# Optimization experiments

Measured on AMD Instinct MI355X. Metric: run time of the kernel, lower is better.

Reference implementation:

```python
import jax, jax.numpy as jnp
import numpy as np

B, C1, C2, N1, N2 = 8, 16, 32, 256, 128


def _masks():
    # static numpy masks, mirroring EquivariantLayer.__init__
    n_max, n_min = max(N1, N2), min(N1, N2)
    k = np.arange(n_max)
    k[k > n_max // 2] -= n_max
    mask = np.abs(k) <= n_min / 2            # |k| <= n_min/2 (both nyquists)
    mask2 = mask[: n_max // 2 + 1].copy()    # taken BEFORE removing neg nyquist
    nyq_pos = k == n_min / 2
    nyq_pos2 = nyq_pos[: n_max // 2 + 1]
    nyq_neg = k == -n_min / 2
    mask[nyq_neg] = False                    # drop negative nyquist row
    return mask, mask2, nyq_pos, nyq_pos2

MASK, MASK2, NYQ_POS, NYQ_POS2 = _masks()


def rot90_kernel(t):
    # 90-deg rotation about grid point [0,0] for periodic kernels:
    # transpose last two dims, keep column 0, reverse remaining columns
    t = jnp.swapaxes(t, -1, -2)
    return jnp.concatenate([t[..., :1], t[..., 1:][..., ::-1]], axis=-1)


def symmetric_kernel(kernel):
    # average over the 8 elements of D4 (rotations + transpose*rotations)
    k1 = kernel
    k2 = rot90_kernel(k1)
    k3 = rot90_kernel(k2)
    k4 = rot90_kernel(k3)
    k5 = jnp.swapaxes(k1, -1, -2)
    k6 = rot90_kernel(k5)
    k7 = rot90_kernel(k6)
    k8 = rot90_kernel(k7)
    return (k1 + k2 + k3 + k4 + k5 + k6 + k7 + k8) / 8.0


def _forward(f, kernel):
    F = jnp.fft.rfft2(f)                                  # [b,c1,N1,N1//2+1]
    # downsample: zero nyquist modes, truncate spectrum, rescale
    F = jnp.where(jnp.asarray(NYQ_POS)[None, None, :, None], 0, F)
    F = jnp.where(jnp.asarray(NYQ_POS2)[None, None, None, :], 0, F)
    F = F[:, :, MASK, :][:, :, :, MASK2] * (N2 / N1) ** 2  # [b,c1,N2,N2//2+1]
    # spectral convolution with D4-symmetrized kernel
    K = jnp.fft.rfft2(symmetric_kernel(kernel))            # [1,c1,c2,N2,N2//2+1]
    conv = jnp.einsum('bcnk,cdnk->bdnk', F, K[0])          # sum over input channels
    return jnp.fft.irfft2(F), jnp.fft.irfft2(conv)


def setup_inputs() -> dict:
    key = jax.random.key(0)
    kf, kk = jax.random.split(key)
    f = jax.random.normal(kf, (B, C1, N1, N1), dtype=jnp.float32)
    eps = 0.1
    kernel = eps * (2.0 * jax.random.uniform(kk, (1, C1, C2, N2, N2), dtype=jnp.float32) - 1.0)
    return {"f": f, "kernel": kernel}


def reference(f, kernel):
    return _forward(f, kernel)
```

## Files before the change

### kernel.cpp

```cpp
#include <hip/hip_runtime.h>

#define PI_F 3.14159265358979f

typedef unsigned int  uint32;
typedef unsigned short ushort16;

__device__ __forceinline__ float2 cmul(float2 a, float2 b) {
    return make_float2(a.x * b.x - a.y * b.y, a.x * b.y + a.y * b.x);
}
__device__ __forceinline__ float2 cadd(float2 a, float2 b) { return make_float2(a.x + b.x, a.y + b.y); }
__device__ __forceinline__ float2 csub(float2 a, float2 b) { return make_float2(a.x - b.x, a.y - b.y); }
__device__ __forceinline__ float2 shflx(float2 v, int m) {
    return make_float2(__shfl_xor(v.x, m, 64), __shfl_xor(v.y, m, 64));
}
__device__ __forceinline__ float2 shfli(float2 v, int src) {
    return make_float2(__shfl(v.x, src, 64), __shfl(v.y, src, 64));
}
__device__ __forceinline__ int brev6(int x) { return (int)(__brev((unsigned)x) >> 26); }

__device__ __forceinline__ uint32 bfu(float x) {
    uint32 u = __float_as_uint(x);
    return (u + 0x7FFFu + ((u >> 16) & 1u)) >> 16;
}
__device__ __forceinline__ uint32 packbf2(float2 v) { return bfu(v.x) | (bfu(v.y) << 16); }
__device__ __forceinline__ float2 unpackbf2(uint32 u) {
    return make_float2(__uint_as_float(u << 16), __uint_as_float(u & 0xFFFF0000u));
}
__device__ __forceinline__ float bf2f(ushort16 u) { return __uint_as_float((uint32)u << 16); }

template<int CTRL>
__device__ __forceinline__ float dpp1(float x) {
    return __builtin_bit_cast(float, __builtin_amdgcn_update_dpp(
        0, __builtin_bit_cast(int, x), CTRL, 0xF, 0xF, true));
}
template<int CTRL>
__device__ __forceinline__ float2 dppx(float2 v) {
    return make_float2(dpp1<CTRL>(v.x), dpp1<CTRL>(v.y));
}

__device__ __forceinline__ float swz4(float x) {
    return __int_as_float(__builtin_amdgcn_ds_swizzle(__float_as_int(x), 0x101F));
}

template<bool INV>
__device__ __forceinline__ void tw_init(int lane, float2* w, float* sg) {
#pragma unroll
    for (int t = 0; t < 6; ++t) {
        int m = 32 >> t;
        bool up = (lane & m) != 0;
        int pos = lane & (m - 1);
        float ang = (INV ? PI_F : -PI_F) * (float)pos / (float)m;
        float sn, cs;
        __sincosf(ang, &sn, &cs);
        w[t]  = up ? make_float2(cs, sn) : make_float2(1.f, 0.f);
        sg[t] = (t < 2) ? (up ? -2.f : 0.f) : (up ? -1.f : 1.f);
    }
}

__device__ __forceinline__ float2 fft64s(float2 v, const float2* w, const float* sg) {
#if __has_builtin(__builtin_amdgcn_permlane32_swap) && __has_builtin(__builtin_amdgcn_permlane16_swap)
    {
        auto rx = __builtin_amdgcn_permlane32_swap(__float_as_uint(v.x), __float_as_uint(v.x), false, false);
        auto ry = __builtin_amdgcn_permlane32_swap(__float_as_uint(v.y), __float_as_uint(v.y), false, false);
        float2 d = make_float2(
            fmaf(sg[0], v.x, __uint_as_float(rx[0]) + __uint_as_float(rx[1])),
            fmaf(sg[0], v.y, __uint_as_float(ry[0]) + __uint_as_float(ry[1])));
        v = cmul(d, w[0]);
    }
    {
        auto rx = __builtin_amdgcn_permlane16_swap(__float_as_uint(v.x), __float_as_uint(v.x), false, false);
        auto ry = __builtin_amdgcn_permlane16_swap(__float_as_uint(v.y), __float_as_uint(v.y), false, false);
        float2 d = make_float2(
            fmaf(sg[1], v.x, __uint_as_float(rx[0]) + __uint_as_float(rx[1])),
            fmaf(sg[1], v.y, __uint_as_float(ry[0]) + __uint_as_float(ry[1])));
        v = cmul(d, w[1]);
    }
#else
    {
        float2 p = shflx(v, 32); float s0 = 1.0f + sg[0];
        float2 d = make_float2(fmaf(s0, v.x, p.x), fmaf(s0, v.y, p.y));
        v = cmul(d, w[0]);
    }
    {
        float2 p = shflx(v, 16); float s1 = 1.0f + sg[1];
        float2 d = make_float2(fmaf(s1, v.x, p.x), fmaf(s1, v.y, p.y));
        v = cmul(d, w[1]);
    }
#endif
    {
        float2 p = dppx<0x128>(v);
        float2 d = make_float2(fmaf(sg[2], v.x, p.x), fmaf(sg[2], v.y, p.y));
        v = cmul(d, w[2]);
    }
    {
        float2 p = make_float2(swz4(v.x), swz4(v.y));
        float2 d = make_float2(fmaf(sg[3], v.x, p.x), fmaf(sg[3], v.y, p.y));
        v = cmul(d, w[3]);
    }
    {
        float2 p = dppx<0x4E>(v);
        float2 d = make_float2(fmaf(sg[4], v.x, p.x), fmaf(sg[4], v.y, p.y));
        v = cmul(d, w[4]);
    }
    {
        float2 p = dppx<0xB1>(v);
        float2 d = make_float2(fmaf(sg[5], v.x, p.x), fmaf(sg[5], v.y, p.y));
        v = cmul(d, w[5]);
    }
    return v;
}

__device__ void kfft_body(const float* __restrict__ kin, ushort16* __restrict__ kout,
                          float2* X, int img) {
    int lane = threadIdx.x & 63, wv = threadIdx.x >> 6;
    float2 w[6]; float sg[6];
    tw_init<false>(lane, w, sg);
    int b6 = brev6(lane);
    float sn, cs;
    __sincosf(-PI_F * (float)lane * (1.0f / 64.0f), &sn, &cs);
    float2 w64 = make_float2(cs, sn);
    __sincosf(-PI_F * (float)b6 * (1.0f / 64.0f), &sn, &cs);
    float2 wub = make_float2(cs, sn);
    const float2* in2 = (const float2*)(kin + (size_t)img * 16384);
    int gm2 = brev6((64 - b6) & 63);
#pragma unroll 2
    for (int rr = 0; rr < 16; ++rr) {
        int r = wv * 16 + rr;
        float2 z = in2[r * 64 + lane];
        z = fft64s(z, w, sg);
        float2 zm = shfli(z, gm2);
        float ar = z.x + zm.x, ai = z.y - zm.y;
        float br = z.x - zm.x, bi = z.y + zm.y;
        float p = wub.x * br - wub.y * bi, q = wub.x * bi + wub.y * br;
        X[r * 65 + b6] = make_float2(0.5f * (ar + q), 0.5f * (ai - p));
    }
    __syncthreads();
    float2 c0[8], c1[8];
#pragma unroll
    for (int cc = 0; cc < 8; ++cc) {
        int k = wv * 8 + cc;
        c0[cc] = X[lane * 65 + k];
        c1[cc] = X[(lane + 64) * 65 + k];
    }
    __syncthreads();
    float* Rr = (float*)X;
#pragma unroll
    for (int cc = 0; cc < 8; ++cc) {
        int k = wv * 8 + cc;
        float2 r0 = c0[cc], r1 = c1[cc];
        float2 t = r0;
        r0 = cadd(t, r1);
        r1 = cmul(csub(t, r1), w64);
        r0 = fft64s(r0, w, sg);
        r1 = fft64s(r1, w, sg);
        Rr[(2 * b6) * 65 + k]     = r0.x;
        Rr[(2 * b6 + 1) * 65 + k] = r1.x;
    }
    __syncthreads();
    ushort4* ko4 = (ushort4*)(kout + (size_t)img * 8192);
    for (int i = threadIdx.x; i < 2048; i += 512) {
        int n = i >> 4, k4 = (i & 15) << 2;
        float op[4];
#pragma unroll
        for (int m = 0; m < 4; ++m) {
            int k = k4 + m;
            float t1 = Rr[n * 65 + k];
            float t2 = Rr[((128 - n) & 127) * 65 + k];
            float t3, t4;
            if (n < 64) {
                t3 = Rr[k * 65 + n];
                t4 = Rr[((128 - k) & 127) * 65 + n];
            } else {
                int c2 = 128 - n; if (c2 > 63) c2 = 63;
                t3 = Rr[((128 - k) & 127) * 65 + c2];
                t4 = Rr[k * 65 + c2];
            }
            op[m] = 0.25f * (t1 + t2 + t3 + t4);
        }
        ushort4 o4;
        o4.x = (ushort16)bfu(op[0]); o4.y = (ushort16)bfu(op[1]);
        o4.z = (ushort16)bfu(op[2]); o4.w = (ushort16)bfu(op[3]);
        ko4[i] = o4;
    }
}

__device__ void rfft_body(const float* __restrict__ f, uint32* __restrict__ G, int bid) {
    int lane = threadIdx.x & 63, wv = threadIdx.x >> 6;
    int row0 = (bid * 8 + wv) * 8;
    float2 w[6]; float sg[6];
    tw_init<false>(lane, w, sg);
    int m = brev6(lane);
    float sn, cs;
    __sincosf(-PI_F * (float)lane * (1.0f / 64.0f), &sn, &cs);
    float2 w64 = make_float2(cs, sn);
    __sincosf(-PI_F * (float)(2 * m) * (1.0f / 128.0f), &sn, &cs);
    float2 wue = make_float2(cs, sn);
    __sincosf(-PI_F * (float)(2 * m + 1) * (1.0f / 128.0f), &sn, &cs);
    float2 wuo = make_float2(cs, sn);
    int src_e = brev6((64 - m) & 63);
    int src_o = brev6(63 - m);
    bool active = (lane & 1) == 0;
#pragma unroll 2
    for (int rr = 0; rr < 8; ++rr) {
        size_t row = (size_t)(row0 + rr);
        const float2* x = (const float2*)(f + row * 256);
        float2 r0 = x[lane], r1 = x[lane + 64];
        float2 t = r0;
        r0 = cadd(t, r1);
        r1 = cmul(csub(t, r1), w64);
        r0 = fft64s(r0, w, sg);
        r1 = fft64s(r1, w, sg);
        float2 zme = shfli(r0, src_e);
        float2 zmo = shfli(r1, src_o);
        float ar = r0.x + zme.x, ai = r0.y - zme.y;
        float br = r0.x - zme.x, bi = r0.y + zme.y;
        float p = wue.x * br - wue.y * bi, q = wue.x * bi + wue.y * br;
        uint32 xe = packbf2(make_float2(0.5f * (ar + q), 0.5f * (ai - p)));
        ar = r1.x + zmo.x; ai = r1.y - zmo.y;
        br = r1.x - zmo.x; bi = r1.y + zmo.y;
        p = wuo.x * br - wuo.y * bi; q = wuo.x * bi + wuo.y * br;
        uint32 xo = packbf2(make_float2(0.5f * (ar + q), 0.5f * (ai - p)));
        if (active) ((uint2*)(G + row * 64))[m] = make_uint2(xe, xo);
    }
}

__global__ __launch_bounds__(512) void mega_a(const float* __restrict__ kin,
                                              ushort16* __restrict__ Kr,
                                              const float* __restrict__ f,
                                              uint32* __restrict__ G) {
    __shared__ float2 SH[128 * 65];
    int bid = blockIdx.x;
    if (bid < 512) kfft_body(kin, Kr, SH, bid);
    else           rfft_body(f, G, bid - 512);
}

__global__ __launch_bounds__(512) void fcolk(const uint32* __restrict__ G,
                                             uint32* __restrict__ FH) {
    __shared__ uint32 S[256 * 17];
    int img = blockIdx.x >> 2, qg = blockIdx.x & 3;
    int lane = threadIdx.x & 63, wv = threadIdx.x >> 6;
    float2 w[6]; float sg[6];
    tw_init<false>(lane, w, sg);
    float sn, cs;
    __sincosf(-PI_F * (float)lane * (1.0f / 64.0f), &sn, &cs);
    float2 w64 = make_float2(cs, sn);
    __sincosf(-PI_F * (float)lane * (1.0f / 128.0f), &sn, &cs);
    float2 w128a = make_float2(cs, sn);
    __sincosf(-PI_F * (float)(lane + 64) * (1.0f / 128.0f), &sn, &cs);
    float2 w128b = make_float2(cs, sn);
    const uint32* src = G + (size_t)img * 16384 + qg * 16;
    for (int i = threadIdx.x; i < 4096; i += 512) {
        int r = i >> 4, c = i & 15;
        S[r * 17 + c] = src[(size_t)r * 64 + c];
    }
    __syncthreads();
    float2 q0[2], q1[2], q2[2], q3[2];
#pragma unroll
    for (int cc = 0; cc < 2; ++cc) {
        int c = wv * 2 + cc;
        q0[cc] = unpackbf2(S[(lane)       * 17 + c]);
        q1[cc] = unpackbf2(S[(lane +  64) * 17 + c]);
        q2[cc] = unpackbf2(S[(lane + 128) * 17 + c]);
        q3[cc] = unpackbf2(S[(lane + 192) * 17 + c]);
    }
    __syncthreads();
    int b6 = brev6(lane);
#pragma unroll
    for (int cc = 0; cc < 2; ++cc) {
        int c = wv * 2 + cc;
        float2 r0 = q0[cc], r1 = q1[cc], r2 = q2[cc], r3 = q3[cc], t;
        t = r0; r0 = cadd(t, r2); r2 = cmul(csub(t, r2), w128a);
        t = r1; r1 = cadd(t, r3); r3 = cmul(csub(t, r3), w128b);
        t = r0; r0 = cadd(t, r1); r1 = cmul(csub(t, r1), w64);
        t = r2; r2 = cadd(t, r3); r3 = cmul(csub(t, r3), w64);
        r0 = fft64s(r0, w, sg); r1 = fft64s(r1, w, sg);
        r2 = fft64s(r2, w, sg); r3 = fft64s(r3, w, sg);
        float2 vv[4] = { r0, r2, r1, r3 };
#pragma unroll
        for (int j = 0; j < 4; ++j) {
            int n = 4 * b6 + j;
            int r = (n < 64) ? n : ((n >= 193) ? n - 128 : -1);
            if (r >= 0)
                S[r * 17 + c] = packbf2(make_float2(vv[j].x * 0.25f, vv[j].y * 0.25f));
        }
    }
    __syncthreads();
    uint32* dst = FH + (size_t)img * 8192 + qg * 16;
    for (int i = threadIdx.x; i < 2048; i += 512) {
        int r = i >> 4, c = i & 15;
        dst[(size_t)r * 64 + c] = (r == 64) ? 0u : S[r * 17 + c];
    }
}

__device__ void einsum_body(const uint32* __restrict__ F, const ushort16* __restrict__ K,
                            uint32* __restrict__ C, uint32* Ft, int bid) {
    int nk0 = bid * 32;
    int t = threadIdx.x;
    for (int i = t; i < 4096; i += 512) {
        int bc = i >> 5, nl = i & 31;
        Ft[i] = F[(size_t)bc * 8192 + nk0 + nl];
    }
    __syncthreads();
    int nl = t & 31, dg = t >> 5;
    int nk = nk0 + nl;
    float2 acc[2][8] = {};
#pragma unroll
    for (int c = 0; c < 16; ++c) {
        float2 fv[8];
#pragma unroll
        for (int b = 0; b < 8; ++b) fv[b] = unpackbf2(Ft[(b * 16 + c) * 32 + nl]);
#pragma unroll
        for (int j = 0; j < 2; ++j) {
            int d = j * 16 + dg;
            float kv = bf2f(K[(size_t)(c * 32 + d) * 8192 + nk]);
#pragma unroll
            for (int b = 0; b < 8; ++b) {
                acc[j][b].x = fmaf(fv[b].x, kv, acc[j][b].x);
                acc[j][b].y = fmaf(fv[b].y, kv, acc[j][b].y);
            }
        }
    }
#pragma unroll
    for (int j = 0; j < 2; ++j) {
        int d = j * 16 + dg;
#pragma unroll
        for (int b = 0; b < 8; ++b)
            C[(size_t)(b * 32 + d) * 8192 + nk] = packbf2(acc[j][b]);
    }
}

__device__ void ifuse_body(const uint32* __restrict__ src, float2* __restrict__ dst,
                           float2* S) {
    int lane = threadIdx.x & 63, wv = threadIdx.x >> 6;
    float2 w[6]; float sg[6];
    tw_init<true>(lane, w, sg);
    float sn, cs;
    __sincosf(PI_F * (float)lane * (1.0f / 64.0f), &sn, &cs);
    float2 w64 = make_float2(cs, sn);
    for (int i = threadIdx.x; i < 8192; i += 512) {
        int r = i >> 6, c = i & 63;
        S[r * 65 + c] = unpackbf2(src[i]);
    }
    __syncthreads();
    float2 c0[8], c1[8];
#pragma unroll
    for (int cc = 0; cc < 8; ++cc) {
        int k = wv * 8 + cc;
        c0[cc] = S[lane * 65 + k];
        c1[cc] = S[(lane + 64) * 65 + k];
    }
    __syncthreads();
    int b6 = brev6(lane);
#pragma unroll
    for (int cc = 0; cc < 8; ++cc) {
        int k = wv * 8 + cc;
        float2 r0 = c0[cc], r1 = c1[cc];
        float2 t = r0;
        r0 = cadd(t, r1);
        r1 = cmul(csub(t, r1), w64);
        r0 = fft64s(r0, w, sg);
        r1 = fft64s(r1, w, sg);
        S[(2 * b6) * 65 + k]     = r0;
        S[(2 * b6 + 1) * 65 + k] = r1;
    }
    __syncthreads();
#pragma unroll 2
    for (int rr = 0; rr < 16; ++rr) {
        int m = wv * 16 + rr;
        float2 X = S[m * 65 + lane];
        float2 Xm = shfli(X, (64 - lane) & 63);
        if (lane == 0) Xm = make_float2(0.f, 0.f);
        float er = 0.5f * (X.x + Xm.x), ei = 0.5f * (X.y - Xm.y);
        float br = 0.5f * (X.x - Xm.x), bi = 0.5f * (X.y + Xm.y);
        float orr = w64.x * br - w64.y * bi, oi = w64.x * bi + w64.y * br;
        float2 Z = make_float2(er - oi, ei + orr);
        Z = fft64s(Z, w, sg);
        dst[m * 64 + b6] = make_float2(Z.x * (1.0f / 8192.0f), Z.y * (1.0f / 8192.0f));
    }
}

__global__ __launch_bounds__(512) void mega2(const uint32* __restrict__ FH,
                                             const ushort16* __restrict__ Kr,
                                             uint32* __restrict__ CONV,
                                             float* __restrict__ out) {
    __shared__ float2 SH[128 * 65];
    int bid = blockIdx.x;
    if (bid < 256) einsum_body(FH, Kr, CONV, (uint32*)SH, bid);
    else {
        int img = bid - 256;
        ifuse_body(FH + (size_t)img * 8192, (float2*)(out + (size_t)img * 16384), SH);
    }
}

__global__ __launch_bounds__(512) void ifuse1(const uint32* __restrict__ CV,
                                              float* __restrict__ out1) {
    __shared__ float2 SH[128 * 65];
    int img = blockIdx.x;
    ifuse_body(CV + (size_t)img * 8192, (float2*)(out1 + (size_t)img * 16384), SH);
}

extern "C" void kernel_launch(void* const* d_in, const int* in_sizes, int n_in,
                              void* d_out, int out_size, void* d_ws, size_t ws_size,
                              hipStream_t stream) {
    const float* f   = (const float*)d_in[0];
    const float* kin = (const float*)d_in[1];
    float* out = (float*)d_out;
    char* ws = (char*)d_ws;

    uint32*   G    = (uint32*)ws;
    uint32*   CONV = (uint32*)ws;
    uint32*   FHAT = (uint32*)(ws + 8388608);
    ushort16* Kr   = (ushort16*)(ws + 16777216);

    mega_a<<<1024, 512, 0, stream>>>(kin, Kr, f, G);
    fcolk<<<512, 512, 0, stream>>>(G, FHAT);
    mega2<<<384, 512, 0, stream>>>(FHAT, Kr, CONV, out);
    ifuse1<<<256, 512, 0, stream>>>(CONV, out + 2097152);
}
```

Before: 161.6 us.

## Fuse row and column input FFTs per image and move to 1024-thread blocks

The separate row-rFFT and column-FFT kernels for the input become one block per image that keeps the intermediate spectrum in a swizzled shared-memory tile. This removes one launch and the global round trip through the intermediate buffer. All kernels switch from 512 to 1024 threads per block, so each wave handles half as many rows or columns, and the einsum gives each thread a single output channel. The cost is fewer blocks for the input FFT stage (128 images), more shared memory per block, and possibly lower occupancy.

```diff
diff --git a/kernel.cpp b/kernel.cpp
--- a/kernel.cpp
+++ b/kernel.cpp
@@ -76,13 +76,11 @@
         v = cmul(d, w[1]);
     }
 #else
-    {
-        float2 p = shflx(v, 32); float s0 = 1.0f + sg[0];
+    {   float2 p = shflx(v, 32); float s0 = 1.0f + sg[0];
         float2 d = make_float2(fmaf(s0, v.x, p.x), fmaf(s0, v.y, p.y));
         v = cmul(d, w[0]);
     }
-    {
-        float2 p = shflx(v, 16); float s1 = 1.0f + sg[1];
+    {   float2 p = shflx(v, 16); float s1 = 1.0f + sg[1];
         float2 d = make_float2(fmaf(s1, v.x, p.x), fmaf(s1, v.y, p.y));
         v = cmul(d, w[1]);
     }
@@ -108,6 +106,10 @@
         v = cmul(d, w[5]);
     }
     return v;
+}
+
+__device__ __forceinline__ int s66(int r, int c) {
+    return r * 66 + (c ^ (((r >> 4) & 3) << 4));
 }
 
 __device__ void kfft_body(const float* __restrict__ kin, ushort16* __restrict__ kout,
@@ -124,8 +126,8 @@
     const float2* in2 = (const float2*)(kin + (size_t)img * 16384);
     int gm2 = brev6((64 - b6) & 63);
 #pragma unroll 2
-    for (int rr = 0; rr < 16; ++rr) {
-        int r = wv * 16 + rr;
+    for (int rr = 0; rr < 8; ++rr) {
+        int r = wv * 8 + rr;
         float2 z = in2[r * 64 + lane];
         z = fft64s(z, w, sg);
         float2 zm = shfli(z, gm2);
@@ -135,18 +137,18 @@
         X[r * 65 + b6] = make_float2(0.5f * (ar + q), 0.5f * (ai - p));
     }
     __syncthreads();
-    float2 c0[8], c1[8];
-#pragma unroll
-    for (int cc = 0; cc < 8; ++cc) {
-        int k = wv * 8 + cc;
+    float2 c0[4], c1[4];
+#pragma unroll
+    for (int cc = 0; cc < 4; ++cc) {
+        int k = wv * 4 + cc;
         c0[cc] = X[lane * 65 + k];
         c1[cc] = X[(lane + 64) * 65 + k];
     }
     __syncthreads();
     float* Rr = (float*)X;
 #pragma unroll
-    for (int cc = 0; cc < 8; ++cc) {
-        int k = wv * 8 + cc;
+    for (int cc = 0; cc < 4; ++cc) {
+        int k = wv * 4 + cc;
         float2 r0 = c0[cc], r1 = c1[cc];
         float2 t = r0;
         r0 = cadd(t, r1);
@@ -158,7 +160,7 @@
     }
     __syncthreads();
     ushort4* ko4 = (ushort4*)(kout + (size_t)img * 8192);
-    for (int i = threadIdx.x; i < 2048; i += 512) {
+    for (int i = threadIdx.x; i < 2048; i += 1024) {
         int n = i >> 4, k4 = (i & 15) << 2;
         float op[4];
 #pragma unroll
@@ -184,15 +186,15 @@
     }
 }
 
-__device__ void rfft_body(const float* __restrict__ f, uint32* __restrict__ G, int bid) {
+__device__ void ffull_body(const float* __restrict__ f, uint32* __restrict__ FH,
+                           uint32* S, int img) {
     int lane = threadIdx.x & 63, wv = threadIdx.x >> 6;
-    int row0 = (bid * 8 + wv) * 8;
     float2 w[6]; float sg[6];
     tw_init<false>(lane, w, sg);
-    int m = brev6(lane);
     float sn, cs;
     __sincosf(-PI_F * (float)lane * (1.0f / 64.0f), &sn, &cs);
     float2 w64 = make_float2(cs, sn);
+    int m = brev6(lane);
     __sincosf(-PI_F * (float)(2 * m) * (1.0f / 128.0f), &sn, &cs);
     float2 wue = make_float2(cs, sn);
     __sincosf(-PI_F * (float)(2 * m + 1) * (1.0f / 128.0f), &sn, &cs);
@@ -200,10 +202,11 @@
     int src_e = brev6((64 - m) & 63);
     int src_o = brev6(63 - m);
     bool active = (lane & 1) == 0;
+    const float* fimg = f + (size_t)img * 65536;
 #pragma unroll 2
-    for (int rr = 0; rr < 8; ++rr) {
-        size_t row = (size_t)(row0 + rr);
-        const float2* x = (const float2*)(f + row * 256);
+    for (int rr = 0; rr < 16; ++rr) {
+        int r = wv * 16 + rr;
+        const float2* x = (const float2*)(fimg + r * 256);
         float2 r0 = x[lane], r1 = x[lane + 64];
         float2 t = r0;
         r0 = cadd(t, r1);
@@ -220,113 +223,90 @@
         br = r1.x - zmo.x; bi = r1.y + zmo.y;
         p = wuo.x * br - wuo.y * bi; q = wuo.x * bi + wuo.y * br;
         uint32 xo = packbf2(make_float2(0.5f * (ar + q), 0.5f * (ai - p)));
-        if (active) ((uint2*)(G + row * 64))[m] = make_uint2(xe, xo);
-    }
-}
-
-__global__ __launch_bounds__(512) void mega_a(const float* __restrict__ kin,
-                                              ushort16* __restrict__ Kr,
-                                              const float* __restrict__ f,
-                                              uint32* __restrict__ G) {
-    __shared__ float2 SH[128 * 65];
-    int bid = blockIdx.x;
-    if (bid < 512) kfft_body(kin, Kr, SH, bid);
-    else           rfft_body(f, G, bid - 512);
-}
-
-__global__ __launch_bounds__(512) void fcolk(const uint32* __restrict__ G,
-                                             uint32* __restrict__ FH) {
-    __shared__ uint32 S[256 * 17];
-    int img = blockIdx.x >> 2, qg = blockIdx.x & 3;
-    int lane = threadIdx.x & 63, wv = threadIdx.x >> 6;
-    float2 w[6]; float sg[6];
-    tw_init<false>(lane, w, sg);
-    float sn, cs;
-    __sincosf(-PI_F * (float)lane * (1.0f / 64.0f), &sn, &cs);
-    float2 w64 = make_float2(cs, sn);
+        if (active) *(uint2*)&S[s66(r, 2 * m)] = make_uint2(xe, xo);
+    }
+    __syncthreads();
     __sincosf(-PI_F * (float)lane * (1.0f / 128.0f), &sn, &cs);
     float2 w128a = make_float2(cs, sn);
     __sincosf(-PI_F * (float)(lane + 64) * (1.0f / 128.0f), &sn, &cs);
     float2 w128b = make_float2(cs, sn);
-    const uint32* src = G + (size_t)img * 16384 + qg * 16;
-    for (int i = threadIdx.x; i < 4096; i += 512) {
-        int r = i >> 4, c = i & 15;
-        S[r * 17 + c] = src[(size_t)r * 64 + c];
-    }
-    __syncthreads();
-    float2 q0[2], q1[2], q2[2], q3[2];
-#pragma unroll
-    for (int cc = 0; cc < 2; ++cc) {
-        int c = wv * 2 + cc;
-        q0[cc] = unpackbf2(S[(lane)       * 17 + c]);
-        q1[cc] = unpackbf2(S[(lane +  64) * 17 + c]);
-        q2[cc] = unpackbf2(S[(lane + 128) * 17 + c]);
-        q3[cc] = unpackbf2(S[(lane + 192) * 17 + c]);
-    }
-    __syncthreads();
     int b6 = brev6(lane);
 #pragma unroll
-    for (int cc = 0; cc < 2; ++cc) {
-        int c = wv * 2 + cc;
-        float2 r0 = q0[cc], r1 = q1[cc], r2 = q2[cc], r3 = q3[cc], t;
-        t = r0; r0 = cadd(t, r2); r2 = cmul(csub(t, r2), w128a);
-        t = r1; r1 = cadd(t, r3); r3 = cmul(csub(t, r3), w128b);
-        t = r0; r0 = cadd(t, r1); r1 = cmul(csub(t, r1), w64);
-        t = r2; r2 = cadd(t, r3); r3 = cmul(csub(t, r3), w64);
-        r0 = fft64s(r0, w, sg); r1 = fft64s(r1, w, sg);
-        r2 = fft64s(r2, w, sg); r3 = fft64s(r3, w, sg);
-        float2 vv[4] = { r0, r2, r1, r3 };
-#pragma unroll
-        for (int j = 0; j < 4; ++j) {
-            int n = 4 * b6 + j;
-            int r = (n < 64) ? n : ((n >= 193) ? n - 128 : -1);
-            if (r >= 0)
-                S[r * 17 + c] = packbf2(make_float2(vv[j].x * 0.25f, vv[j].y * 0.25f));
+    for (int ch = 0; ch < 2; ++ch) {
+        float2 q0[2], q1[2], q2[2], q3[2];
+#pragma unroll
+        for (int cc = 0; cc < 2; ++cc) {
+            int c = wv * 4 + ch * 2 + cc;
+            q0[cc] = unpackbf2(S[s66(lane,       c)]);
+            q1[cc] = unpackbf2(S[s66(lane +  64, c)]);
+            q2[cc] = unpackbf2(S[s66(lane + 128, c)]);
+            q3[cc] = unpackbf2(S[s66(lane + 192, c)]);
         }
-    }
-    __syncthreads();
-    uint32* dst = FH + (size_t)img * 8192 + qg * 16;
-    for (int i = threadIdx.x; i < 2048; i += 512) {
-        int r = i >> 4, c = i & 15;
-        dst[(size_t)r * 64 + c] = (r == 64) ? 0u : S[r * 17 + c];
-    }
+#pragma unroll
+        for (int cc = 0; cc < 2; ++cc) {
+            int c = wv * 4 + ch * 2 + cc;
+            float2 r0 = q0[cc], r1 = q1[cc], r2 = q2[cc], r3 = q3[cc], t;
+            t = r0; r0 = cadd(t, r2); r2 = cmul(csub(t, r2), w128a);
+            t = r1; r1 = cadd(t, r3); r3 = cmul(csub(t, r3), w128b);
+            t = r0; r0 = cadd(t, r1); r1 = cmul(csub(t, r1), w64);
+            t = r2; r2 = cadd(t, r3); r3 = cmul(csub(t, r3), w64);
+            r0 = fft64s(r0, w, sg); r1 = fft64s(r1, w, sg);
+            r2 = fft64s(r2, w, sg); r3 = fft64s(r3, w, sg);
+            float2 vv[4] = { r0, r2, r1, r3 };
+#pragma unroll
+            for (int j = 0; j < 4; ++j) {
+                int n = 4 * b6 + j;
+                int r = (n < 64) ? n : ((n >= 193) ? n - 128 : -1);
+                if (r >= 0)
+                    S[s66(r, c)] = packbf2(make_float2(vv[j].x * 0.25f, vv[j].y * 0.25f));
+            }
+        }
+    }
+    __syncthreads();
+    uint32* dst = FH + (size_t)img * 8192;
+    for (int i = threadIdx.x; i < 8192; i += 1024) {
+        int r = i >> 6, c = i & 63;
+        dst[i] = (r == 64) ? 0u : S[s66(r, c)];
+    }
+}
+
+__global__ __launch_bounds__(1024, 8) void mega_a(const float* __restrict__ kin,
+                                                  ushort16* __restrict__ Kr,
+                                                  const float* __restrict__ f,
+                                                  uint32* __restrict__ FH) {
+    __shared__ uint32 SH[256 * 66];
+    int bid = blockIdx.x;
+    if (bid < 128) ffull_body(f, FH, SH, bid);
+    else           kfft_body(kin, Kr, (float2*)SH, bid - 128);
 }
 
 __device__ void einsum_body(const uint32* __restrict__ F, const ushort16* __restrict__ K,
                             uint32* __restrict__ C, uint32* Ft, int bid) {
     int nk0 = bid * 32;
     int t = threadIdx.x;
-    for (int i = t; i < 4096; i += 512) {
+    for (int i = t; i < 4096; i += 1024) {
         int bc = i >> 5, nl = i & 31;
         Ft[i] = F[(size_t)bc * 8192 + nk0 + nl];
     }
     __syncthreads();
-    int nl = t & 31, dg = t >> 5;
+    int nl = t & 31, d = t >> 5;
     int nk = nk0 + nl;
-    float2 acc[2][8] = {};
+    float2 acc[8] = {};
 #pragma unroll
     for (int c = 0; c < 16; ++c) {
         float2 fv[8];
 #pragma unroll
         for (int b = 0; b < 8; ++b) fv[b] = unpackbf2(Ft[(b * 16 + c) * 32 + nl]);
-#pragma unroll
-        for (int j = 0; j < 2; ++j) {
-            int d = j * 16 + dg;
-            float kv = bf2f(K[(size_t)(c * 32 + d) * 8192 + nk]);
-#pragma unroll
-            for (int b = 0; b < 8; ++b) {
-                acc[j][b].x = fmaf(fv[b].x, kv, acc[j][b].x);
-                acc[j][b].y = fmaf(fv[b].y, kv, acc[j][b].y);
-            }
+        float kv = bf2f(K[(size_t)(c * 32 + d) * 8192 + nk]);
+#pragma unroll
+        for (int b = 0; b < 8; ++b) {
+            acc[b].x = fmaf(fv[b].x, kv, acc[b].x);
+            acc[b].y = fmaf(fv[b].y, kv, acc[b].y);
         }
     }
 #pragma unroll
-    for (int j = 0; j < 2; ++j) {
-        int d = j * 16 + dg;
-#pragma unroll
-        for (int b = 0; b < 8; ++b)
-            C[(size_t)(b * 32 + d) * 8192 + nk] = packbf2(acc[j][b]);
-    }
+    for (int b = 0; b < 8; ++b)
+        C[(size_t)(b * 32 + d) * 8192 + nk] = packbf2(acc[b]);
 }
 
 __device__ void ifuse_body(const uint32* __restrict__ src, float2* __restrict__ dst,
@@ -337,24 +317,17 @@
     float sn, cs;
     __sincosf(PI_F * (float)lane * (1.0f / 64.0f), &sn, &cs);
     float2 w64 = make_float2(cs, sn);
-    for (int i = threadIdx.x; i < 8192; i += 512) {
+    for (int i = threadIdx.x; i < 8192; i += 1024) {
         int r = i >> 6, c = i & 63;
         S[r * 65 + c] = unpackbf2(src[i]);
     }
     __syncthreads();
-    float2 c0[8], c1[8];
-#pragma unroll
-    for (int cc = 0; cc < 8; ++cc) {
-        int k = wv * 8 + cc;
-        c0[cc] = S[lane * 65 + k];
-        c1[cc] = S[(lane + 64) * 65 + k];
-    }
-    __syncthreads();
     int b6 = brev6(lane);
 #pragma unroll
-    for (int cc = 0; cc < 8; ++cc) {
-        int k = wv * 8 + cc;
-        float2 r0 = c0[cc], r1 = c1[cc];
+    for (int cc = 0; cc < 4; ++cc) {
+        int k = wv * 4 + cc;
+        float2 r0 = S[lane * 65 + k];
+        float2 r1 = S[(lane + 64) * 65 + k];
         float2 t = r0;
         r0 = cadd(t, r1);
         r1 = cmul(csub(t, r1), w64);
@@ -365,8 +338,8 @@
     }
     __syncthreads();
 #pragma unroll 2
-    for (int rr = 0; rr < 16; ++rr) {
-        int m = wv * 16 + rr;
+    for (int rr = 0; rr < 8; ++rr) {
+        int m = wv * 8 + rr;
         float2 X = S[m * 65 + lane];
         float2 Xm = shfli(X, (64 - lane) & 63);
         if (lane == 0) Xm = make_float2(0.f, 0.f);
@@ -379,10 +352,10 @@
     }
 }
 
-__global__ __launch_bounds__(512) void mega2(const uint32* __restrict__ FH,
-                                             const ushort16* __restrict__ Kr,
-                                             uint32* __restrict__ CONV,
-                                             float* __restrict__ out) {
+__global__ __launch_bounds__(1024, 8) void mega2(const uint32* __restrict__ FH,
+                                                 const ushort16* __restrict__ Kr,
+                                                 uint32* __restrict__ CONV,
+                                                 float* __restrict__ out) {
     __shared__ float2 SH[128 * 65];
     int bid = blockIdx.x;
     if (bid < 256) einsum_body(FH, Kr, CONV, (uint32*)SH, bid);
@@ -392,8 +365,8 @@
     }
 }
 
-__global__ __launch_bounds__(512) void ifuse1(const uint32* __restrict__ CV,
-                                              float* __restrict__ out1) {
+__global__ __launch_bounds__(1024, 8) void ifuse1(const uint32* __restrict__ CV,
+                                                  float* __restrict__ out1) {
     __shared__ float2 SH[128 * 65];
     int img = blockIdx.x;
     ifuse_body(CV + (size_t)img * 8192, (float2*)(out1 + (size_t)img * 16384), SH);
@@ -407,13 +380,11 @@
     float* out = (float*)d_out;
     char* ws = (char*)d_ws;
 
-    uint32*   G    = (uint32*)ws;
     uint32*   CONV = (uint32*)ws;
     uint32*   FHAT = (uint32*)(ws + 8388608);
     ushort16* Kr   = (ushort16*)(ws + 16777216);
 
-    mega_a<<<1024, 512, 0, stream>>>(kin, Kr, f, G);
-    fcolk<<<512, 512, 0, stream>>>(G, FHAT);
-    mega2<<<384, 512, 0, stream>>>(FHAT, Kr, CONV, out);
-    ifuse1<<<256, 512, 0, stream>>>(CONV, out + 2097152);
-}
+    mega_a<<<640, 1024, 0, stream>>>(kin, Kr, f, FHAT);
+    mega2<<<384, 1024, 0, stream>>>(FHAT, Kr, CONV, out);
+    ifuse1<<<256, 1024, 0, stream>>>(CONV, out + 2097152);
+}
```

New measurement: 218.6 us. 1.35x slower.
